# Kernel tuning notes

Hardware: AMD Instinct MI355X
Metric: run time of the kernel (lower is better)

The kernel has to match this reference:

```python
import jax, jax.numpy as jnp
import numpy as np

SCALING_FACTOR = 1.8
K = 10
ALPHA = 0.15
EPS = 1e-12


def setup_inputs() -> dict:
    key = jax.random.key(0)
    k1, k2, k3, k4 = jax.random.split(key, 4)
    N, E, IN, OUT = 100000, 3200000, 512, 256
    x = jax.random.normal(k1, (N, IN), dtype=jnp.float32)
    edge_index = jax.random.randint(k2, (2, E), 0, N, dtype=jnp.int64)
    W1 = jax.random.normal(k3, (OUT, IN), dtype=jnp.float32) * (1.0 / np.sqrt(IN))
    b1 = jax.random.normal(k4, (OUT,), dtype=jnp.float32) * 0.01
    return {"x": x, "edge_index": edge_index, "W1": W1, "b1": b1}


def _gcn_norm(edge_index, num_nodes):
    # add self-loops (PyG gcn_norm default), symmetric D^-1/2 (A+I) D^-1/2
    loops = jnp.arange(num_nodes, dtype=edge_index.dtype)
    src = jnp.concatenate([edge_index[0], loops])
    dst = jnp.concatenate([edge_index[1], loops])
    deg = jax.ops.segment_sum(jnp.ones_like(dst, dtype=jnp.float32), dst,
                              num_segments=num_nodes)
    dinv = jnp.where(deg > 0, jax.lax.rsqrt(deg), 0.0)
    norm = dinv[src] * dinv[dst]  # [E+N]
    return src, dst, norm


def reference(x, edge_index, W1, b1):
    N = x.shape[0]
    # linear1
    h = jnp.einsum('ni,oi->no', x, W1) + b1  # [N, OUT]
    # F.normalize(p=2, dim=1) * scaling_factor
    nrm = jnp.sqrt(jnp.sum(h * h, axis=1, keepdims=True))
    h = h / jnp.maximum(nrm, EPS) * SCALING_FACTOR
    # APPNP K=10, alpha=0.15
    src, dst, norm = _gcn_norm(edge_index, N)
    h0 = h

    def step(z, _):
        msg = z[src] * norm[:, None]                       # gather + scale
        agg = jax.ops.segment_sum(msg, dst, num_segments=N)  # scatter-add
        z = (1.0 - ALPHA) * agg + ALPHA * h0
        return z, None

    z, _ = jax.lax.scan(step, h, None, length=K)
    return z
```

## Files before the change

kernel.cpp:

```cpp
#include <hip/hip_runtime.h>
#include <hip/hip_fp16.h>


#define ALPHA 0.15f
#define BETA 0.85f
#define SCALE 1.8f

typedef _Float16 f16x8 __attribute__((ext_vector_type(8)));
typedef float f32x4 __attribute__((ext_vector_type(4)));

__global__ void convert_w(const float* __restrict__ W1, _Float16* __restrict__ Wh) {
    int i = blockIdx.x * blockDim.x + threadIdx.x;
    if (i < 256 * 512) Wh[i] = (_Float16)W1[i];
}

__global__ __launch_bounds__(256) void gemm_f16(
    const float* __restrict__ A, const _Float16* __restrict__ Wh,
    const float* __restrict__ bias, float* __restrict__ C, int M) {
    __shared__ _Float16 As[64][72];
    const int tid  = threadIdx.x;
    const int wv   = tid >> 6;
    const int lane = tid & 63;
    const int lc   = lane & 15;
    const int lr   = lane >> 4;
    const int m0   = blockIdx.x * 64;
    const int n0w  = wv * 64;

    f32x4 acc[4][4];
#pragma unroll
    for (int i = 0; i < 4; i++)
#pragma unroll
        for (int j = 0; j < 4; j++) {
            acc[i][j][0] = 0.f; acc[i][j][1] = 0.f;
            acc[i][j][2] = 0.f; acc[i][j][3] = 0.f;
        }

    const int srow = tid >> 2;
    const int sseg = tid & 3;
    const bool inb = (m0 + srow) < M;

    for (int k0 = 0; k0 < 512; k0 += 64) {
        float4 av0, av1, av2, av3;
        if (inb) {
            const float4* ap = (const float4*)(A + (size_t)(m0 + srow) * 512 + k0 + sseg * 16);
            av0 = ap[0]; av1 = ap[1]; av2 = ap[2]; av3 = ap[3];
        } else {
            av0 = av1 = av2 = av3 = make_float4(0.f, 0.f, 0.f, 0.f);
        }
        if (k0) __syncthreads();
        f16x8 p0, p1;
        p0[0] = (_Float16)av0.x; p0[1] = (_Float16)av0.y;
        p0[2] = (_Float16)av0.z; p0[3] = (_Float16)av0.w;
        p0[4] = (_Float16)av1.x; p0[5] = (_Float16)av1.y;
        p0[6] = (_Float16)av1.z; p0[7] = (_Float16)av1.w;
        p1[0] = (_Float16)av2.x; p1[1] = (_Float16)av2.y;
        p1[2] = (_Float16)av2.z; p1[3] = (_Float16)av2.w;
        p1[4] = (_Float16)av3.x; p1[5] = (_Float16)av3.y;
        p1[6] = (_Float16)av3.z; p1[7] = (_Float16)av3.w;
        _Float16* wp = &As[srow][sseg * 16];
        *(f16x8*)wp = p0;
        *(f16x8*)(wp + 8) = p1;
        __syncthreads();

        f16x8 bf[2][4];
#pragma unroll
        for (int s = 0; s < 2; ++s)
#pragma unroll
            for (int nt = 0; nt < 4; ++nt)
                bf[s][nt] = *(const f16x8*)(Wh + (size_t)(n0w + nt * 16 + lc) * 512
                                            + k0 + s * 32 + lr * 8);

#pragma unroll
        for (int s = 0; s < 2; ++s) {
            f16x8 af[4];
#pragma unroll
            for (int mt = 0; mt < 4; ++mt)
                af[mt] = *(const f16x8*)&As[mt * 16 + lc][s * 32 + lr * 8];
#pragma unroll
            for (int mt = 0; mt < 4; ++mt)
#pragma unroll
                for (int nt = 0; nt < 4; ++nt)
                    acc[mt][nt] = __builtin_amdgcn_mfma_f32_16x16x32_f16(
                        af[mt], bf[s][nt], acc[mt][nt], 0, 0, 0);
        }
    }

    float bv[4];
#pragma unroll
    for (int nt = 0; nt < 4; ++nt) bv[nt] = bias[n0w + nt * 16 + lc];
#pragma unroll
    for (int mt = 0; mt < 4; ++mt)
#pragma unroll
        for (int r = 0; r < 4; ++r) {
            int m = m0 + mt * 16 + lr * 4 + r;
            if (m < M) {
                float* cp = C + (size_t)m * 256 + n0w + lc;
#pragma unroll
                for (int nt = 0; nt < 4; ++nt)
                    cp[nt * 16] = acc[mt][nt][r] + bv[nt];
            }
        }
}

__global__ __launch_bounds__(256) void normalize_kernel(
    const float* __restrict__ h, const float* __restrict__ dinv,
    __half* __restrict__ h16, __half* __restrict__ y0, int N) {
    int n = blockIdx.x;
    if (n >= N) return;
    int t = threadIdx.x;
    float v = h[(size_t)n * 256 + t];
    float ss = v * v;
#pragma unroll
    for (int off = 32; off > 0; off >>= 1) ss += __shfl_down(ss, off, 64);
    __shared__ float wsum[4];
    int w = t >> 6, lane = t & 63;
    if (lane == 0) wsum[w] = ss;
    __syncthreads();
    float tot = wsum[0] + wsum[1] + wsum[2] + wsum[3];
    float nrm = sqrtf(tot);
    float s = SCALE / fmaxf(nrm, 1e-12f);
    float hv = v * s;
    h16[(size_t)n * 256 + t] = __float2half(hv);
    y0[(size_t)n * 256 + t] = __float2half(hv * dinv[n]);
}

__global__ void init_counts(int* __restrict__ counts, int N) {
    int i = blockIdx.x * blockDim.x + threadIdx.x;
    if (i < N) counts[i] = 1;
}

__global__ __launch_bounds__(256) void count_xcd(
    const int* __restrict__ dst, int* __restrict__ counts, int E, int N) {
    const int b = blockIdx.x, x = b & 7, c = b >> 3;
    const int NC = gridDim.x >> 3;
    const int lo = (int)(((long long)x * N) >> 3);
    const int hi = (int)(((long long)(x + 1) * N) >> 3);
    const int csz = (((E + NC - 1) / NC) + 3) & ~3;
    const int e0 = c * csz;
    const int e1 = min(e0 + csz, E);
    const int rem = (e1 > e0) ? (e1 - e0) : 0;
    const int t = threadIdx.x;
    const int nvec = ((E & 3) == 0) ? (rem >> 2) : 0;
    for (int i = t; i < nvec; i += 256) {
        const int e = e0 + (i << 2);
        int4 d4 = *(const int4*)(dst + e);
        if (d4.x >= lo && d4.x < hi) atomicAdd(&counts[d4.x], 1);
        if (d4.y >= lo && d4.y < hi) atomicAdd(&counts[d4.y], 1);
        if (d4.z >= lo && d4.z < hi) atomicAdd(&counts[d4.z], 1);
        if (d4.w >= lo && d4.w < hi) atomicAdd(&counts[d4.w], 1);
    }
    for (int e = e0 + (nvec << 2) + t; e < e1; e += 256) {
        int d = dst[e];
        if (d >= lo && d < hi) atomicAdd(&counts[d], 1);
    }
}

__global__ void dinv_kernel(const int* __restrict__ counts, float* __restrict__ dinv, int N) {
    int i = blockIdx.x * blockDim.x + threadIdx.x;
    if (i < N) dinv[i] = rsqrtf((float)counts[i]);
}

__global__ __launch_bounds__(256) void scan_phase1(
    const int* __restrict__ counts, int* __restrict__ offsets,
    int* __restrict__ blocksums, int N) {
    __shared__ int sdata[256];
    int b = blockIdx.x;
    int base = b * 1024;
    int t = threadIdx.x;
    int v[4];
    int idx0 = base + t * 4;
    int sum = 0;
#pragma unroll
    for (int j = 0; j < 4; j++) {
        int i = idx0 + j;
        v[j] = (i < N) ? counts[i] : 0;
        sum += v[j];
    }
    sdata[t] = sum;
    __syncthreads();
    for (int off = 1; off < 256; off <<= 1) {
        int x = (t >= off) ? sdata[t - off] : 0;
        __syncthreads();
        sdata[t] += x;
        __syncthreads();
    }
    int incl = sdata[t];
    int excl = incl - sum;
    if (t == 255) blocksums[b] = incl;
    int run = excl;
#pragma unroll
    for (int j = 0; j < 4; j++) {
        int i = idx0 + j;
        if (i < N) offsets[i] = run;
        run += v[j];
    }
}

__global__ __launch_bounds__(128) void scan_phase2(int* __restrict__ blocksums, int nb) {
    __shared__ int s[128];
    int t = threadIdx.x;
    int v = (t < nb) ? blocksums[t] : 0;
    s[t] = v;
    __syncthreads();
    for (int off = 1; off < 128; off <<= 1) {
        int x = (t >= off) ? s[t - off] : 0;
        __syncthreads();
        s[t] += x;
        __syncthreads();
    }
    if (t < nb) blocksums[t] = s[t] - v;
}

__global__ void scan_phase3(int* __restrict__ offsets, const int* __restrict__ blocksums,
                            int* __restrict__ cursor, int N, int total) {
    int i = blockIdx.x * blockDim.x + threadIdx.x;
    if (i < N) {
        int o = offsets[i] + blocksums[i >> 10];
        offsets[i] = o;
        cursor[i] = o;
    }
    if (i == N) offsets[N] = total;
}

__global__ __launch_bounds__(256) void fill_xcd(
    const int* __restrict__ src, const int* __restrict__ dst,
    int* __restrict__ cursor, int* __restrict__ col, int E, int N) {
    const int b = blockIdx.x, x = b & 7, c = b >> 3;
    const int NC = gridDim.x >> 3;
    const int lo = (int)(((long long)x * N) >> 3);
    const int hi = (int)(((long long)(x + 1) * N) >> 3);
    const int csz = (((E + NC - 1) / NC) + 3) & ~3;
    const int e0 = c * csz;
    const int e1 = min(e0 + csz, E);
    const int rem = (e1 > e0) ? (e1 - e0) : 0;
    const int t = threadIdx.x;
    const int nvec = ((E & 3) == 0) ? (rem >> 2) : 0;
    for (int i = t; i < nvec; i += 256) {
        const int e = e0 + (i << 2);
        int4 d4 = *(const int4*)(dst + e);
        if (d4.x >= lo && d4.x < hi) { int p = atomicAdd(&cursor[d4.x], 1); col[p] = src[e]; }
        if (d4.y >= lo && d4.y < hi) { int p = atomicAdd(&cursor[d4.y], 1); col[p] = src[e + 1]; }
        if (d4.z >= lo && d4.z < hi) { int p = atomicAdd(&cursor[d4.z], 1); col[p] = src[e + 2]; }
        if (d4.w >= lo && d4.w < hi) { int p = atomicAdd(&cursor[d4.w], 1); col[p] = src[e + 3]; }
    }
    for (int e = e0 + (nvec << 2) + t; e < e1; e += 256) {
        int d = dst[e];
        if (d >= lo && d < hi) { int p = atomicAdd(&cursor[d], 1); col[p] = src[e]; }
    }
    if (c == 0) {
        for (int n = lo + t; n < hi; n += 256) {
            int p = atomicAdd(&cursor[n], 1);
            col[p] = n;
        }
    }
}

__device__ __forceinline__ void acc_half4(float4& a, float2 r) {
    union { float2 f; __half2 h[2]; } u;
    u.f = r;
    float2 lo = __half22float2(u.h[0]);
    float2 hi = __half22float2(u.h[1]);
    a.x += lo.x; a.y += lo.y; a.z += hi.x; a.w += hi.y;
}

template <bool FINAL>
__global__ __launch_bounds__(256) void spmm_kernel(
    const __half* __restrict__ yin, const __half* __restrict__ h16,
    const int* __restrict__ offs, const int* __restrict__ col,
    const float* __restrict__ dinv, void* __restrict__ outp, int N) {
    int gw = blockIdx.x * 4 + (threadIdx.x >> 6);
    if (gw >= N) return;
    int lane = threadIdx.x & 63;
    int beg = offs[gw], end = offs[gw + 1];

    float4 a0 = make_float4(0.f, 0.f, 0.f, 0.f);
    float4 a1 = make_float4(0.f, 0.f, 0.f, 0.f);
    float4 a2 = make_float4(0.f, 0.f, 0.f, 0.f);
    float4 a3 = make_float4(0.f, 0.f, 0.f, 0.f);

    int e = beg;
    for (; e + 3 < end; e += 4) {
        int s0 = __builtin_nontemporal_load(col + e);
        int s1 = __builtin_nontemporal_load(col + e + 1);
        int s2 = __builtin_nontemporal_load(col + e + 2);
        int s3 = __builtin_nontemporal_load(col + e + 3);
        float2 r0 = ((const float2*)(yin + (size_t)s0 * 256))[lane];
        float2 r1 = ((const float2*)(yin + (size_t)s1 * 256))[lane];
        float2 r2 = ((const float2*)(yin + (size_t)s2 * 256))[lane];
        float2 r3 = ((const float2*)(yin + (size_t)s3 * 256))[lane];
        acc_half4(a0, r0); acc_half4(a1, r1); acc_half4(a2, r2); acc_half4(a3, r3);
    }
    for (; e < end; ++e) {
        int s0 = __builtin_nontemporal_load(col + e);
        float2 r0 = ((const float2*)(yin + (size_t)s0 * 256))[lane];
        acc_half4(a0, r0);
    }

    float dg = dinv[gw];
    float wd = BETA * dg;

    const float* hp = (const float*)(h16 + (size_t)gw * 256) + lane * 2;
    float hx = __builtin_nontemporal_load(hp);
    float hy = __builtin_nontemporal_load(hp + 1);
    float4 hh;
    {
        union { float f; __half2 h; } ux, uy;
        ux.f = hx; uy.f = hy;
        float2 lo = __half22float2(ux.h);
        float2 hi = __half22float2(uy.h);
        hh.x = lo.x; hh.y = lo.y; hh.z = hi.x; hh.w = hi.y;
    }

    float4 o;
    o.x = wd * (a0.x + a1.x + a2.x + a3.x) + ALPHA * hh.x;
    o.y = wd * (a0.y + a1.y + a2.y + a3.y) + ALPHA * hh.y;
    o.z = wd * (a0.z + a1.z + a2.z + a3.z) + ALPHA * hh.z;
    o.w = wd * (a0.w + a1.w + a2.w + a3.w) + ALPHA * hh.w;

    if (FINAL) {
        float* op = (float*)outp + (size_t)gw * 256 + lane * 4;
        __builtin_nontemporal_store(o.x, op);
        __builtin_nontemporal_store(o.y, op + 1);
        __builtin_nontemporal_store(o.z, op + 2);
        __builtin_nontemporal_store(o.w, op + 3);
    } else {
        __half2 p0 = __floats2half2_rn(o.x * dg, o.y * dg);
        __half2 p1 = __floats2half2_rn(o.z * dg, o.w * dg);
        union { float f; __half2 h; } u0, u1;
        u0.h = p0; u1.h = p1;
        float* op = (float*)((__half*)outp + (size_t)gw * 256) + lane * 2;
        __builtin_nontemporal_store(u0.f, op);
        __builtin_nontemporal_store(u1.f, op + 1);
    }
}

extern "C" void kernel_launch(void* const* d_in, const int* in_sizes, int n_in,
                              void* d_out, int out_size, void* d_ws, size_t ws_size,
                              hipStream_t stream) {
    const float* x  = (const float*)d_in[0];
    const int* ei   = (const int*)d_in[1];
    const float* W1 = (const float*)d_in[2];
    const float* b1 = (const float*)d_in[3];
    float* out = (float*)d_out;

    const int N = in_sizes[0] / 512;
    const int E = in_sizes[1] / 2;
    const int* src = ei;
    const int* dst = ei + E;
    const int NNZ = E + N;

    char* w = (char*)d_ws;
    float* h0 = (float*)w;      w += (size_t)N * 256 * 4;
    __half* h16 = (__half*)w;   w += (size_t)N * 256 * 2;
    __half* y0 = (__half*)w;    w += (size_t)N * 256 * 2;
    __half* yB = (__half*)w;    w += (size_t)N * 256 * 2;
    _Float16* Wh = (_Float16*)w; w += (size_t)256 * 512 * 2;
    float* dinv = (float*)w;    w += (size_t)N * 4;
    int* counts = (int*)w;      w += (size_t)N * 4;
    int* offsets = (int*)w;     w += (size_t)(N + 64) * 4;
    int* blocksums = (int*)w;   w += 128 * 4;
    int* col = (int*)w;         w += (size_t)NNZ * 4;
    __half* yA = (__half*)h0;

    init_counts<<<(N + 255) / 256, 256, 0, stream>>>(counts, N);
    count_xcd<<<512, 256, 0, stream>>>(dst, counts, E, N);
    dinv_kernel<<<(N + 255) / 256, 256, 0, stream>>>(counts, dinv, N);
    convert_w<<<(256 * 512 + 255) / 256, 256, 0, stream>>>(W1, Wh);
    gemm_f16<<<(N + 63) / 64, 256, 0, stream>>>(x, Wh, b1, h0, N);
    normalize_kernel<<<N, 256, 0, stream>>>(h0, dinv, h16, y0, N);
    int nb = (N + 1023) / 1024;
    scan_phase1<<<nb, 256, 0, stream>>>(counts, offsets, blocksums, N);
    scan_phase2<<<1, 128, 0, stream>>>(blocksums, nb);
    scan_phase3<<<(N + 256) / 256, 256, 0, stream>>>(offsets, blocksums, counts, N, NNZ);
    fill_xcd<<<512, 256, 0, stream>>>(src, dst, counts, col, E, N);
    int nblk = (N + 3) / 4;
    const __half* cur = y0;
    for (int it = 0; it < 9; ++it) {
        __half* nxt = (it & 1) ? yB : yA;
        spmm_kernel<false><<<nblk, 256, 0, stream>>>(cur, h16, offsets, col, dinv,
                                                     (void*)nxt, N);
        cur = nxt;
    }
    spmm_kernel<true><<<nblk, 256, 0, stream>>>(cur, h16, offsets, col, dinv,
                                                (void*)out, N);
}
```

Before: 3.165 ms.

## Split SpMM wavefront into half-waves gathering two neighbor rows with 16-byte loads

The SpMM kernel now has each half-wave of 32 lanes fetch a whole 512-byte fp16 neighbor row with float4 loads, so one wave gathers two neighbor rows per instruction instead of one row with 8-byte loads. Column indices are loaded cooperatively, 16 at a time, and broadcast with shuffles, with the next batch prefetched. The two half-wave partial sums are combined with a cross-half xor-shuffle before the epilogue. This cuts the number of gather instructions and scalar index loads, at the cost of extra shuffles, remainder-handling complexity, and a padded col buffer for the prefetch overrun.

```diff
diff --git a/kernel.cpp b/kernel.cpp
--- a/kernel.cpp
+++ b/kernel.cpp
@@ -255,12 +255,15 @@
     }
 }
 
-__device__ __forceinline__ void acc_half4(float4& a, float2 r) {
-    union { float2 f; __half2 h[2]; } u;
+__device__ __forceinline__ void acc_h8(float4& a, float4& b, float4 r) {
+    union { float4 f; __half2 h[4]; } u;
     u.f = r;
-    float2 lo = __half22float2(u.h[0]);
-    float2 hi = __half22float2(u.h[1]);
-    a.x += lo.x; a.y += lo.y; a.z += hi.x; a.w += hi.y;
+    float2 v0 = __half22float2(u.h[0]);
+    float2 v1 = __half22float2(u.h[1]);
+    float2 v2 = __half22float2(u.h[2]);
+    float2 v3 = __half22float2(u.h[3]);
+    a.x += v0.x; a.y += v0.y; a.z += v1.x; a.w += v1.y;
+    b.x += v2.x; b.y += v2.y; b.z += v3.x; b.w += v3.y;
 }
 
 template <bool FINAL>
@@ -268,57 +271,80 @@
     const __half* __restrict__ yin, const __half* __restrict__ h16,
     const int* __restrict__ offs, const int* __restrict__ col,
     const float* __restrict__ dinv, void* __restrict__ outp, int N) {
-    int gw = blockIdx.x * 4 + (threadIdx.x >> 6);
+    const int gw = blockIdx.x * 4 + (threadIdx.x >> 6);
     if (gw >= N) return;
-    int lane = threadIdx.x & 63;
-    int beg = offs[gw], end = offs[gw + 1];
-
-    float4 a0 = make_float4(0.f, 0.f, 0.f, 0.f);
-    float4 a1 = make_float4(0.f, 0.f, 0.f, 0.f);
-    float4 a2 = make_float4(0.f, 0.f, 0.f, 0.f);
-    float4 a3 = make_float4(0.f, 0.f, 0.f, 0.f);
+    const int lane = threadIdx.x & 63;
+    const int hb = lane >> 5;
+    const int hl = lane & 31;
+    const int beg = offs[gw], end = offs[gw + 1];
+
+    float4 accA[2], accB[2];
+#pragma unroll
+    for (int j = 0; j < 2; ++j) {
+        accA[j] = make_float4(0.f, 0.f, 0.f, 0.f);
+        accB[j] = make_float4(0.f, 0.f, 0.f, 0.f);
+    }
 
     int e = beg;
-    for (; e + 3 < end; e += 4) {
-        int s0 = __builtin_nontemporal_load(col + e);
-        int s1 = __builtin_nontemporal_load(col + e + 1);
-        int s2 = __builtin_nontemporal_load(col + e + 2);
-        int s3 = __builtin_nontemporal_load(col + e + 3);
-        float2 r0 = ((const float2*)(yin + (size_t)s0 * 256))[lane];
-        float2 r1 = ((const float2*)(yin + (size_t)s1 * 256))[lane];
-        float2 r2 = ((const float2*)(yin + (size_t)s2 * 256))[lane];
-        float2 r3 = ((const float2*)(yin + (size_t)s3 * 256))[lane];
-        acc_half4(a0, r0); acc_half4(a1, r1); acc_half4(a2, r2); acc_half4(a3, r3);
-    }
-    for (; e < end; ++e) {
-        int s0 = __builtin_nontemporal_load(col + e);
-        float2 r0 = ((const float2*)(yin + (size_t)s0 * 256))[lane];
-        acc_half4(a0, r0);
-    }
-
-    float dg = dinv[gw];
-    float wd = BETA * dg;
-
-    const float* hp = (const float*)(h16 + (size_t)gw * 256) + lane * 2;
-    float hx = __builtin_nontemporal_load(hp);
-    float hy = __builtin_nontemporal_load(hp + 1);
+    int c = 0;
+    if (e + 15 < end) c = col[e + (lane & 15)];
+    while (e + 15 < end) {
+        int cn = col[e + 16 + (lane & 15)];
+        float4 r[8];
+#pragma unroll
+        for (int j = 0; j < 8; ++j) {
+            int s = __shfl(c, 2 * j + hb, 64);
+            r[j] = ((const float4*)(yin + (size_t)s * 256))[hl];
+        }
+#pragma unroll
+        for (int j = 0; j < 8; ++j) acc_h8(accA[j & 1], accB[j & 1], r[j]);
+        c = cn;
+        e += 16;
+    }
+    for (; e + 1 < end; e += 2) {
+        int s = col[e + hb];
+        float4 r = ((const float4*)(yin + (size_t)s * 256))[hl];
+        acc_h8(accA[0], accB[0], r);
+    }
+    if (e < end) {
+        int s = col[e];
+        float4 r = ((const float4*)(yin + (size_t)s * 256))[hl];
+        if (hb == 0) acc_h8(accA[1], accB[1], r);
+    }
+
+    float4 sA, sB;
+    sA.x = accA[0].x + accA[1].x; sA.y = accA[0].y + accA[1].y;
+    sA.z = accA[0].z + accA[1].z; sA.w = accA[0].w + accA[1].w;
+    sB.x = accB[0].x + accB[1].x; sB.y = accB[0].y + accB[1].y;
+    sB.z = accB[0].z + accB[1].z; sB.w = accB[0].w + accB[1].w;
+
+    float4 own  = hb ? sB : sA;
+    float4 send = hb ? sA : sB;
+    own.x += __shfl_xor(send.x, 32);
+    own.y += __shfl_xor(send.y, 32);
+    own.z += __shfl_xor(send.z, 32);
+    own.w += __shfl_xor(send.w, 32);
+
+    const float dg = dinv[gw];
+    const float wd = BETA * dg;
+
     float4 hh;
     {
-        union { float f; __half2 h; } ux, uy;
-        ux.f = hx; uy.f = hy;
-        float2 lo = __half22float2(ux.h);
-        float2 hi = __half22float2(uy.h);
-        hh.x = lo.x; hh.y = lo.y; hh.z = hi.x; hh.w = hi.y;
+        union { float2 f; __half2 h[2]; } uh;
+        uh.f = *(const float2*)((const __half*)h16 + (size_t)gw * 256 + hl * 8 + hb * 4);
+        float2 h01 = __half22float2(uh.h[0]);
+        float2 h23 = __half22float2(uh.h[1]);
+        hh.x = h01.x; hh.y = h01.y; hh.z = h23.x; hh.w = h23.y;
     }
 
     float4 o;
-    o.x = wd * (a0.x + a1.x + a2.x + a3.x) + ALPHA * hh.x;
-    o.y = wd * (a0.y + a1.y + a2.y + a3.y) + ALPHA * hh.y;
-    o.z = wd * (a0.z + a1.z + a2.z + a3.z) + ALPHA * hh.z;
-    o.w = wd * (a0.w + a1.w + a2.w + a3.w) + ALPHA * hh.w;
+    o.x = wd * own.x + ALPHA * hh.x;
+    o.y = wd * own.y + ALPHA * hh.y;
+    o.z = wd * own.z + ALPHA * hh.z;
+    o.w = wd * own.w + ALPHA * hh.w;
 
     if (FINAL) {
-        float* op = (float*)outp + (size_t)gw * 256 + lane * 4;
+        float* op = (float*)outp + (size_t)gw * 256 + hl * 8 + hb * 4;
         __builtin_nontemporal_store(o.x, op);
         __builtin_nontemporal_store(o.y, op + 1);
         __builtin_nontemporal_store(o.z, op + 2);
@@ -326,11 +352,9 @@
     } else {
         __half2 p0 = __floats2half2_rn(o.x * dg, o.y * dg);
         __half2 p1 = __floats2half2_rn(o.z * dg, o.w * dg);
-        union { float f; __half2 h; } u0, u1;
-        u0.h = p0; u1.h = p1;
-        float* op = (float*)((__half*)outp + (size_t)gw * 256) + lane * 2;
-        __builtin_nontemporal_store(u0.f, op);
-        __builtin_nontemporal_store(u1.f, op + 1);
+        union { float2 f; __half2 h[2]; } u;
+        u.h[0] = p0; u.h[1] = p1;
+        *(float2*)((__half*)outp + (size_t)gw * 256 + hl * 8 + hb * 4) = u.f;
     }
 }
 
@@ -359,7 +383,7 @@
     int* counts = (int*)w;      w += (size_t)N * 4;
     int* offsets = (int*)w;     w += (size_t)(N + 64) * 4;
     int* blocksums = (int*)w;   w += 128 * 4;
-    int* col = (int*)w;         w += (size_t)NNZ * 4;
+    int* col = (int*)w;         w += (size_t)(NNZ + 64) * 4;
     __half* yA = (__half*)h0;
 
     init_counts<<<(N + 255) / 256, 256, 0, stream>>>(counts, N);
```

Result: faster. 3.020 ms (-4.6%).
